# Performance work log

Measured on AMD Instinct MI355X. Metric: run time of the kernel, lower is better.

Reference implementation:

```python
import jax, jax.numpy as jnp
import numpy as np
import math

HIDDEN = 768
NUM_HEADS = 12
HEAD_DIM = HIDDEN // NUM_HEADS
EPS = 1e-05
MU_LEARNED = 0.0    # registered buffer init value (inference mode)
SIGMA_LEARNED = 1.0 # registered buffer init value (inference mode)
SCALES = (0.5, 1.0, 2.0)


def make_pe(n, d):
    # Sinusoidal positional encoding, identical to PositionalEncoding buffer.
    pos = np.arange(n, dtype=np.float32)[:, None]
    div = np.exp(np.arange(0, d, 2, dtype=np.float32) * (-math.log(10000.0) / d))
    pe = np.zeros((n, d), dtype=np.float32)
    pe[:, 0::2] = np.sin(pos * div)
    pe[:, 1::2] = np.cos(pos * div)
    return jnp.asarray(pe)


def setup_inputs() -> dict:
    key = jax.random.key(0)
    ks = jax.random.split(key, 12)
    B, C, Hh, Ww = 8, 256, 32, 32
    feat = jax.random.normal(ks[0], (B, C, Hh, Ww), jnp.float32)
    I = jax.random.uniform(ks[1], (B, 1, Hh, Ww), jnp.float32)
    sc_c = 1.0 / math.sqrt(C)
    sd = 1.0 / math.sqrt(HIDDEN)
    proj_w = jax.random.normal(ks[2], (C, HIDDEN), jnp.float32) * sc_c  # 1x1 conv as matmul
    proj_b = jnp.zeros((HIDDEN,), jnp.float32)
    wq = jax.random.normal(ks[3], (HIDDEN, HIDDEN), jnp.float32) * sd
    bq = jnp.zeros((HIDDEN,), jnp.float32)
    wk = jax.random.normal(ks[4], (HIDDEN, HIDDEN), jnp.float32) * sd
    bk = jnp.zeros((HIDDEN,), jnp.float32)
    wv = jax.random.normal(ks[5], (HIDDEN, HIDDEN), jnp.float32) * sd
    bv = jnp.zeros((HIDDEN,), jnp.float32)
    wo = jax.random.normal(ks[6], (HIDDEN, HIDDEN), jnp.float32) * sd
    bo = jnp.zeros((HIDDEN,), jnp.float32)
    lam = jnp.float32(0.5)
    return dict(feat=feat, I=I, proj_w=proj_w, proj_b=proj_b,
                wq=wq, bq=bq, wk=wk, bk=bk, wv=wv, bv=bv, wo=wo, bo=bo, lam=lam)


def reference(feat, I, proj_w, proj_b, wq, bq, wk, bk, wv, bv, wo, bo, lam):
    B, C, Hh, Ww = feat.shape
    N = Hh * Ww
    # HiddenFeatureProjection: 1x1 conv projection -> flatten -> tokens [B, N, D]
    tokens = jnp.einsum('bchw,cd->bhwd', feat, proj_w).reshape(B, N, HIDDEN) + proj_b
    tokens = tokens + make_pe(N, HIDDEN)[None]
    # GaussianWeightModule (inference path, learned buffers mu=0, sigma=1)
    G = sum(jnp.exp(-(I - MU_LEARNED) ** 2 / (2.0 * (k * SIGMA_LEARNED) ** 2 + EPS))
            for k in SCALES) / float(len(SCALES))  # [B,1,H,W]
    g = G.reshape(B, N)                              # H*W == N by construction
    bias = g[:, :, None] * g[:, None, :]             # [B, N, N] outer product
    # GaussianEnhancedAttention
    q = (tokens @ wq + bq).reshape(B, N, NUM_HEADS, HEAD_DIM).transpose(0, 2, 1, 3)
    k = (tokens @ wk + bk).reshape(B, N, NUM_HEADS, HEAD_DIM).transpose(0, 2, 1, 3)
    v = (tokens @ wv + bv).reshape(B, N, NUM_HEADS, HEAD_DIM).transpose(0, 2, 1, 3)
    scores = jnp.einsum('bhnd,bhmd->bhnm', q, k) / math.sqrt(HEAD_DIM)
    scores = scores + lam * bias[:, None, :, :]
    attn = jax.nn.softmax(scores, axis=-1)
    out = jnp.einsum('bhnm,bhmd->bhnd', attn, v).transpose(0, 2, 1, 3).reshape(B, N, HIDDEN)
    return out @ wo + bo
```

## Files before the change

kernel.cpp:

```cpp
#include <hip/hip_runtime.h>
#include <hip/hip_bf16.h>
#include <math.h>

#define HIDDEN 768
#define NHEADS 12
#define HDIM   64
#define NTOK   1024
#define BATCH  8
#define CIN    256
#define M_ALL  (BATCH * NTOK)
#define LSTR   72

typedef __hip_bfloat16 bf16;
typedef short frag8 __attribute__((ext_vector_type(8)));
typedef float f32x4 __attribute__((ext_vector_type(4)));

#define GL2LDS(gp, lp) \
    __builtin_amdgcn_global_load_lds((const __attribute__((address_space(1))) void*)(gp), \
                                     (__attribute__((address_space(3))) void*)(lp), 16, 0, 0)

__device__ __forceinline__ short f2bs(float x){
    union { bf16 h; short s; } u; u.h = __float2bfloat16(x); return u.s;
}

__device__ __forceinline__ float gaussw(float x){
    float x2 = x * x;
    return (__expf(-x2 / 0.50001f) + __expf(-x2 / 2.00001f) + __expf(-x2 / 8.00001f)) * (1.0f / 3.0f);
}

__global__ __launch_bounds__(256) void prep_all(
    const float* __restrict__ wq, const float* __restrict__ wk,
    const float* __restrict__ wv, const float* __restrict__ wo,
    const float* __restrict__ proj_w, const float* __restrict__ feat,
    short* __restrict__ wtqkv, short* __restrict__ wtp, short* __restrict__ featT)
{
    __shared__ short t[64][65];
    const int blk = blockIdx.x;
    const float* W; short* WT; int K, N, k0, n0;
    if (blk < 576) {
        int p = blk / 144, rem = blk % 144;
        const float* srcs[4] = {wq, wk, wv, wo};
        W = srcs[p]; WT = wtqkv + (size_t)p * HIDDEN * HIDDEN;
        K = HIDDEN; N = HIDDEN; k0 = (rem / 12) * 64; n0 = (rem % 12) * 64;
    } else if (blk < 624) {
        int rem = blk - 576;
        W = proj_w; WT = wtp;
        K = CIN; N = HIDDEN; k0 = (rem / 12) * 64; n0 = (rem % 12) * 64;
    } else {
        int rem = blk - 624;
        int b = rem / 64; rem %= 64;
        W = feat + (size_t)b * CIN * NTOK; WT = featT + (size_t)b * NTOK * CIN;
        K = CIN; N = NTOK; k0 = (rem / 16) * 64; n0 = (rem % 16) * 64;
    }
    const int tid = threadIdx.x;
    #pragma unroll
    for (int it = 0; it < 16; it++) {
        int e = tid + 256 * it;
        int kk = e / 64, nn = e % 64;
        t[kk][nn] = f2bs(W[(size_t)(k0 + kk) * N + n0 + nn]);
    }
    __syncthreads();
    #pragma unroll
    for (int it = 0; it < 16; it++) {
        int e = tid + 256 * it;
        int nn = e / 64, kk = e % 64;
        WT[(size_t)(n0 + nn) * K + k0 + kk] = t[kk][nn];
    }
}

__global__ __launch_bounds__(256) void transpose_v(
    const short* __restrict__ v, short* __restrict__ vT)
{
    __shared__ short t[64][65];
    const int nt = blockIdx.x;
    const int bh = blockIdx.y;
    const int b = bh / NHEADS, h = bh % NHEADS;
    const int tid = threadIdx.x;
    #pragma unroll
    for (int it = 0; it < 16; it++) {
        int e = tid + 256 * it;
        int rr = e / 64, cc = e % 64;
        t[rr][cc] = v[(size_t)(b * NTOK + nt * 64 + rr) * HIDDEN + h * HDIM + cc];
    }
    __syncthreads();
    #pragma unroll
    for (int it = 0; it < 16; it++) {
        int e = tid + 256 * it;
        int c2 = e / 64, r2 = e % 64;
        vT[((size_t)bh * HDIM + c2) * NTOK + nt * 64 + r2] = t[r2][c2];
    }
}

__global__ __launch_bounds__(256) void gemm_mfma128(
    const short* __restrict__ A, const short* __restrict__ WT0, long wt_z,
    const float* __restrict__ b0, const float* __restrict__ b1, const float* __restrict__ b2,
    short* o0, short* o1, short* o2, int K)
{
    __shared__ short Al[128 * 32];
    __shared__ short Bl[128 * 32];
    const int z = blockIdx.z;
    const short* WT  = WT0 + (size_t)z * wt_z;
    const float* bias = (z == 0) ? b0 : (z == 1) ? b1 : b2;
    short* outv       = (z == 0) ? o0 : (z == 1) ? o1 : o2;

    const int tid  = threadIdx.x;
    const int m0   = blockIdx.x * 128;
    const int n0   = blockIdx.y * 128;
    const int lane = tid & 63, wid = tid >> 6;
    const int wm   = (wid >> 1) * 64, wn = (wid & 1) * 64;
    const int l16  = lane & 15, quad = lane >> 4;

    const int sr  = lane >> 2;
    const int ssg = (lane & 3) ^ ((sr >> 1) & 3);
    const int fsw = (l16 >> 1) & 3;

    const f32x4 z4 = {0.f, 0.f, 0.f, 0.f};
    f32x4 acc[4][4];
    #pragma unroll
    for (int i = 0; i < 4; i++)
        #pragma unroll
        for (int j = 0; j < 4; j++) acc[i][j] = z4;

    for (int k0 = 0; k0 < K; k0 += 32) {
        #pragma unroll
        for (int t = 0; t < 2; t++) {
            int rbase = wid * 32 + t * 16;
            int r = rbase + sr;
            GL2LDS(A  + (size_t)(m0 + r) * K + k0 + ssg * 8, &Al[rbase * 32]);
            GL2LDS(WT + (size_t)(n0 + r) * K + k0 + ssg * 8, &Bl[rbase * 32]);
        }
        __syncthreads();
        frag8 af[4], bfr[4];
        #pragma unroll
        for (int i = 0; i < 4; i++)
            af[i]  = *(const frag8*)&Al[(wm + i * 16 + l16) * 32 + ((quad ^ fsw) * 8)];
        #pragma unroll
        for (int j = 0; j < 4; j++)
            bfr[j] = *(const frag8*)&Bl[(wn + j * 16 + l16) * 32 + ((quad ^ fsw) * 8)];
        #pragma unroll
        for (int i = 0; i < 4; i++)
            #pragma unroll
            for (int j = 0; j < 4; j++)
                acc[i][j] = __builtin_amdgcn_mfma_f32_16x16x32_bf16(af[i], bfr[j], acc[i][j], 0, 0, 0);
        __syncthreads();
    }

    #pragma unroll
    for (int i = 0; i < 4; i++) {
        #pragma unroll
        for (int r = 0; r < 4; r++) {
            int m = m0 + wm + i * 16 + quad * 4 + r;
            #pragma unroll
            for (int j = 0; j < 4; j++) {
                int col = n0 + wn + j * 16 + l16;
                outv[(size_t)m * HIDDEN + col] = f2bs(acc[i][j][r] + bias[col]);
            }
        }
    }
}

template<int MODE>
__global__ __launch_bounds__(256) void gemm_mfma64(
    const short* __restrict__ A, const short* __restrict__ WT,
    const float* __restrict__ bias, void* outv, int K)
{
    __shared__ short Al[64 * 32];
    __shared__ short Bl[128 * 32];
    const int tid  = threadIdx.x;
    const int m0   = blockIdx.x * 64;
    const int n0   = blockIdx.y * 128;
    const int lane = tid & 63, wid = tid >> 6;
    const int wn   = wid * 32;
    const int l16  = lane & 15, quad = lane >> 4;

    const int sr  = lane >> 2;
    const int ssg = (lane & 3) ^ ((sr >> 1) & 3);
    const int fsw = (l16 >> 1) & 3;

    const f32x4 z4 = {0.f, 0.f, 0.f, 0.f};
    f32x4 acc[4][2];
    #pragma unroll
    for (int i = 0; i < 4; i++)
        #pragma unroll
        for (int j = 0; j < 2; j++) acc[i][j] = z4;

    for (int k0 = 0; k0 < K; k0 += 32) {
        GL2LDS(A + (size_t)(m0 + wid * 16 + sr) * K + k0 + ssg * 8, &Al[(wid * 16) * 32]);
        #pragma unroll
        for (int t = 0; t < 2; t++) {
            int rbase = wid * 32 + t * 16;
            GL2LDS(WT + (size_t)(n0 + rbase + sr) * K + k0 + ssg * 8, &Bl[rbase * 32]);
        }
        __syncthreads();
        frag8 af[4], bfr[2];
        #pragma unroll
        for (int i = 0; i < 4; i++)
            af[i]  = *(const frag8*)&Al[(i * 16 + l16) * 32 + ((quad ^ fsw) * 8)];
        #pragma unroll
        for (int j = 0; j < 2; j++)
            bfr[j] = *(const frag8*)&Bl[(wn + j * 16 + l16) * 32 + ((quad ^ fsw) * 8)];
        #pragma unroll
        for (int i = 0; i < 4; i++)
            #pragma unroll
            for (int j = 0; j < 2; j++)
                acc[i][j] = __builtin_amdgcn_mfma_f32_16x16x32_bf16(af[i], bfr[j], acc[i][j], 0, 0, 0);
        __syncthreads();
    }

    const float kfac = -9.210340371976184f / 768.0f;
    #pragma unroll
    for (int i = 0; i < 4; i++) {
        #pragma unroll
        for (int r = 0; r < 4; r++) {
            int m = m0 + i * 16 + quad * 4 + r;
            #pragma unroll
            for (int j = 0; j < 2; j++) {
                int col = n0 + wn + j * 16 + l16;
                float val = acc[i][j][r] + bias[col];
                if (MODE == 1) {
                    int n_tok = m & (NTOK - 1);
                    float ang = (float)n_tok * expf((float)(2 * (col >> 1)) * kfac);
                    val += (col & 1) ? cosf(ang) : sinf(ang);
                }
                if (MODE == 2) ((float*)outv)[(size_t)m * HIDDEN + col] = val;
                else           ((short*)outv)[(size_t)m * HIDDEN + col] = f2bs(val);
            }
        }
    }
}

__global__ __launch_bounds__(256, 3) void attn_mfma(
    const short* __restrict__ q, const short* __restrict__ k, const short* __restrict__ vT,
    const float* __restrict__ I, const float* __restrict__ lam_p, short* __restrict__ out)
{
    __shared__ short QP[128 * LSTR];
    __shared__ short Ks[64 * 64];
    __shared__ short Vt[64 * 64];
    __shared__ float gL[NTOK];

    const int tid  = threadIdx.x;
    const int lin  = blockIdx.x;
    const int xcd  = lin & 7, slot = lin >> 3;
    const int b    = xcd;
    const int h    = slot >> 3;
    const int qt   = slot & 7;
    const float L2E  = 1.4426950408889634f;
    const float lam2 = lam_p[0] * L2E;
    const float scl  = 0.125f * L2E;
    const int lane = tid & 63, wave = tid >> 6;
    const int l16  = lane & 15, quad = lane >> 4;

    const int sr   = lane >> 3;
    const int slin = lane & 7;
    const int ssg  = slin ^ sr;
    const int fsw  = l16 & 7;

    for (int i = tid; i < NTOK; i += 256) gL[i] = gaussw(I[b * NTOK + i]);

    #pragma unroll
    for (int it = 0; it < 4; it++) {
        int e = tid + 256 * it;
        int r = e >> 3, seg = e & 7;
        *(frag8*)&QP[r * LSTR + seg * 8] =
            *(const frag8*)&q[(size_t)(b * NTOK + qt * 128 + r) * HIDDEN + h * HDIM + seg * 8];
    }
    __syncthreads();

    frag8 aq[2][2];
    #pragma unroll
    for (int half = 0; half < 2; half++) {
        aq[half][0] = *(const frag8*)&QP[(wave * 32 + half * 16 + l16) * LSTR + quad * 8];
        aq[half][1] = *(const frag8*)&QP[(wave * 32 + half * 16 + l16) * LSTR + 32 + quad * 8];
    }
    float gi[2][4];
    #pragma unroll
    for (int half = 0; half < 2; half++)
        #pragma unroll
        for (int r = 0; r < 4; r++)
            gi[half][r] = gL[qt * 128 + wave * 32 + half * 16 + quad * 4 + r];

    const f32x4 z4 = {0.f, 0.f, 0.f, 0.f};
    f32x4 o_acc[2][4];
    #pragma unroll
    for (int half = 0; half < 2; half++)
        #pragma unroll
        for (int d = 0; d < 4; d++) o_acc[half][d] = z4;
    float l_run[2][4] = {};

    const size_t kb  = (size_t)b * NTOK * HIDDEN + h * HDIM;
    const size_t vtb = (size_t)(b * NHEADS + h) * HDIM * NTOK;

    for (int jt = 0; jt < 16; jt++) {
        __syncthreads();
        #pragma unroll
        for (int t = 0; t < 2; t++) {
            int rbase = wave * 16 + t * 8;
            int r = rbase + sr;
            GL2LDS(k  + kb  + (size_t)(jt * 64 + r) * HIDDEN + ssg * 8, &Ks[rbase * 64]);
            GL2LDS(vT + vtb + (size_t)r * NTOK + jt * 64 + ssg * 8,     &Vt[rbase * 64]);
        }
        __syncthreads();

        float p[2][4][4];
        #pragma unroll
        for (int t4 = 0; t4 < 4; t4++) {
            frag8 bk0 = *(const frag8*)&Ks[(t4 * 16 + l16) * 64 + ((quad ^ fsw) * 8)];
            frag8 bk1 = *(const frag8*)&Ks[(t4 * 16 + l16) * 64 + (((quad + 4) ^ fsw) * 8)];
            #pragma unroll
            for (int half = 0; half < 2; half++) {
                f32x4 a = z4;
                a = __builtin_amdgcn_mfma_f32_16x16x32_bf16(aq[half][0], bk0, a, 0, 0, 0);
                a = __builtin_amdgcn_mfma_f32_16x16x32_bf16(aq[half][1], bk1, a, 0, 0, 0);
                #pragma unroll
                for (int r = 0; r < 4; r++) p[half][t4][r] = a[r];
            }
        }

        float gjs[4];
        #pragma unroll
        for (int t4 = 0; t4 < 4; t4++) gjs[t4] = lam2 * gL[jt * 64 + t4 * 16 + l16];

        #pragma unroll
        for (int half = 0; half < 2; half++)
            #pragma unroll
            for (int t4 = 0; t4 < 4; t4++)
                #pragma unroll
                for (int r = 0; r < 4; r++) {
                    float e = exp2f(p[half][t4][r] * scl + gi[half][r] * gjs[t4]);
                    l_run[half][r] += e;
                    QP[(wave * 32 + half * 16 + quad * 4 + r) * LSTR + t4 * 16 + l16] = f2bs(e);
                }

        frag8 ap[2][2];
        #pragma unroll
        for (int half = 0; half < 2; half++) {
            ap[half][0] = *(const frag8*)&QP[(wave * 32 + half * 16 + l16) * LSTR + quad * 8];
            ap[half][1] = *(const frag8*)&QP[(wave * 32 + half * 16 + l16) * LSTR + 32 + quad * 8];
        }
        #pragma unroll
        for (int d = 0; d < 4; d++) {
            frag8 bv0 = *(const frag8*)&Vt[(d * 16 + l16) * 64 + ((quad ^ fsw) * 8)];
            frag8 bv1 = *(const frag8*)&Vt[(d * 16 + l16) * 64 + (((quad + 4) ^ fsw) * 8)];
            #pragma unroll
            for (int half = 0; half < 2; half++) {
                o_acc[half][d] = __builtin_amdgcn_mfma_f32_16x16x32_bf16(ap[half][0], bv0, o_acc[half][d], 0, 0, 0);
                o_acc[half][d] = __builtin_amdgcn_mfma_f32_16x16x32_bf16(ap[half][1], bv1, o_acc[half][d], 0, 0, 0);
            }
        }
    }

    #pragma unroll
    for (int half = 0; half < 2; half++)
        #pragma unroll
        for (int r = 0; r < 4; r++) {
            float l = l_run[half][r];
            #pragma unroll
            for (int off = 1; off < 16; off <<= 1) l += __shfl_xor(l, off);
            float inv_l = 1.0f / l;
            int row = qt * 128 + wave * 32 + half * 16 + quad * 4 + r;
            #pragma unroll
            for (int d = 0; d < 4; d++)
                out[(size_t)(b * NTOK + row) * HIDDEN + h * HDIM + d * 16 + l16]
                    = f2bs(o_acc[half][d][r] * inv_l);
        }
}

extern "C" void kernel_launch(void* const* d_in, const int* in_sizes, int n_in,
                              void* d_out, int out_size, void* d_ws, size_t ws_size,
                              hipStream_t stream)
{
    const float* feat   = (const float*)d_in[0];
    const float* I      = (const float*)d_in[1];
    const float* proj_w = (const float*)d_in[2];
    const float* proj_b = (const float*)d_in[3];
    const float* wq     = (const float*)d_in[4];
    const float* bq     = (const float*)d_in[5];
    const float* wk     = (const float*)d_in[6];
    const float* bk     = (const float*)d_in[7];
    const float* wv     = (const float*)d_in[8];
    const float* bv     = (const float*)d_in[9];
    const float* wo     = (const float*)d_in[10];
    const float* bo     = (const float*)d_in[11];
    const float* lam    = (const float*)d_in[12];
    float* out = (float*)d_out;

    short* wtqkv = (short*)d_ws;
    short* wto   = wtqkv + (size_t)3 * HIDDEN * HIDDEN;
    short* wtp   = wto   + (size_t)HIDDEN * HIDDEN;
    short* tokens= wtp   + (size_t)HIDDEN * CIN;
    short* qbuf  = tokens+ (size_t)M_ALL * HIDDEN;
    short* featT = qbuf;
    short* vTb   = tokens;
    short* kbuf  = (short*)d_out;
    short* vbuf  = kbuf + (size_t)M_ALL * HIDDEN;

    prep_all<<<1136, 256, 0, stream>>>(wq, wk, wv, wo, proj_w, feat, wtqkv, wtp, featT);
    gemm_mfma64<1><<<dim3(128, 6), 256, 0, stream>>>(featT, wtp, proj_b, tokens, CIN);
    gemm_mfma128<<<dim3(64, 6, 3), 256, 0, stream>>>(tokens, wtqkv, (long)HIDDEN * HIDDEN,
                                                     bq, bk, bv,
                                                     qbuf, kbuf, vbuf, HIDDEN);
    transpose_v<<<dim3(16, 96), 256, 0, stream>>>(vbuf, vTb);
    attn_mfma<<<768, 256, 0, stream>>>(qbuf, kbuf, vTb, I, lam, qbuf);
    gemm_mfma64<2><<<dim3(128, 6), 256, 0, stream>>>(qbuf, wto, bo, out, HIDDEN);
}
```

Measured before the change: 239.8 us.

## Double-buffer K/V tiles in attention and precompute Gaussian weights

```diff
diff --git a/kernel.cpp b/kernel.cpp
--- a/kernel.cpp
+++ b/kernel.cpp
@@ -13,6 +13,7 @@
 
 typedef __hip_bfloat16 bf16;
 typedef short frag8 __attribute__((ext_vector_type(8)));
+typedef short s16x4 __attribute__((ext_vector_type(4)));
 typedef float f32x4 __attribute__((ext_vector_type(4)));
 
 #define GL2LDS(gp, lp) \
@@ -69,8 +70,15 @@
 }
 
 __global__ __launch_bounds__(256) void transpose_v(
-    const short* __restrict__ v, short* __restrict__ vT)
-{
+    const short* __restrict__ v, short* __restrict__ vT,
+    const float* __restrict__ I, float* __restrict__ g)
+{
+    if (blockIdx.y == BATCH * NHEADS) {
+        int idx = blockIdx.x * 512 + threadIdx.x * 2;
+        g[idx]     = gaussw(I[idx]);
+        g[idx + 1] = gaussw(I[idx + 1]);
+        return;
+    }
     __shared__ short t[64][65];
     const int nt = blockIdx.x;
     const int bh = blockIdx.y;
@@ -231,12 +239,11 @@
 
 __global__ __launch_bounds__(256, 3) void attn_mfma(
     const short* __restrict__ q, const short* __restrict__ k, const short* __restrict__ vT,
-    const float* __restrict__ I, const float* __restrict__ lam_p, short* __restrict__ out)
-{
-    __shared__ short QP[128 * LSTR];
-    __shared__ short Ks[64 * 64];
-    __shared__ short Vt[64 * 64];
-    __shared__ float gL[NTOK];
+    const float* __restrict__ g, const float* __restrict__ lam_p, short* __restrict__ out)
+{
+    __shared__ short Pl[128 * LSTR];
+    __shared__ short Ks[2][64 * 64];
+    __shared__ short Vt[2][64 * 64];
 
     const int tid  = threadIdx.x;
     const int lin  = blockIdx.x;
@@ -255,29 +262,30 @@
     const int ssg  = slin ^ sr;
     const int fsw  = l16 & 7;
 
-    for (int i = tid; i < NTOK; i += 256) gL[i] = gaussw(I[b * NTOK + i]);
-
-    #pragma unroll
-    for (int it = 0; it < 4; it++) {
-        int e = tid + 256 * it;
-        int r = e >> 3, seg = e & 7;
-        *(frag8*)&QP[r * LSTR + seg * 8] =
-            *(const frag8*)&q[(size_t)(b * NTOK + qt * 128 + r) * HIDDEN + h * HDIM + seg * 8];
+    const size_t kb  = (size_t)b * NTOK * HIDDEN + h * HDIM;
+    const size_t vtb = (size_t)(b * NHEADS + h) * HDIM * NTOK;
+    const float* gk  = g + b * NTOK;
+
+    frag8 aq[2][2];
+    #pragma unroll
+    for (int half = 0; half < 2; half++)
+        #pragma unroll
+        for (int kc = 0; kc < 2; kc++)
+            aq[half][kc] = *(const frag8*)&q[(size_t)(b * NTOK + qt * 128 + wave * 32 + half * 16 + l16) * HIDDEN
+                                             + h * HDIM + kc * 32 + quad * 8];
+    float gq[2];
+    #pragma unroll
+    for (int half = 0; half < 2; half++)
+        gq[half] = lam2 * gk[qt * 128 + wave * 32 + half * 16 + l16];
+
+    #pragma unroll
+    for (int t = 0; t < 2; t++) {
+        int rbase = wave * 16 + t * 8;
+        int r = rbase + sr;
+        GL2LDS(k  + kb  + (size_t)r * HIDDEN + ssg * 8,  &Ks[0][rbase * 64]);
+        GL2LDS(vT + vtb + (size_t)r * NTOK + ssg * 8,    &Vt[0][rbase * 64]);
     }
     __syncthreads();
-
-    frag8 aq[2][2];
-    #pragma unroll
-    for (int half = 0; half < 2; half++) {
-        aq[half][0] = *(const frag8*)&QP[(wave * 32 + half * 16 + l16) * LSTR + quad * 8];
-        aq[half][1] = *(const frag8*)&QP[(wave * 32 + half * 16 + l16) * LSTR + 32 + quad * 8];
-    }
-    float gi[2][4];
-    #pragma unroll
-    for (int half = 0; half < 2; half++)
-        #pragma unroll
-        for (int r = 0; r < 4; r++)
-            gi[half][r] = gL[qt * 128 + wave * 32 + half * 16 + quad * 4 + r];
 
     const f32x4 z4 = {0.f, 0.f, 0.f, 0.f};
     f32x4 o_acc[2][4];
@@ -285,84 +293,88 @@
     for (int half = 0; half < 2; half++)
         #pragma unroll
         for (int d = 0; d < 4; d++) o_acc[half][d] = z4;
-    float l_run[2][4] = {};
-
-    const size_t kb  = (size_t)b * NTOK * HIDDEN + h * HDIM;
-    const size_t vtb = (size_t)(b * NHEADS + h) * HDIM * NTOK;
+    float l_run[2] = {0.f, 0.f};
 
     for (int jt = 0; jt < 16; jt++) {
-        __syncthreads();
-        #pragma unroll
-        for (int t = 0; t < 2; t++) {
-            int rbase = wave * 16 + t * 8;
-            int r = rbase + sr;
-            GL2LDS(k  + kb  + (size_t)(jt * 64 + r) * HIDDEN + ssg * 8, &Ks[rbase * 64]);
-            GL2LDS(vT + vtb + (size_t)r * NTOK + jt * 64 + ssg * 8,     &Vt[rbase * 64]);
-        }
-        __syncthreads();
+        const int cur = jt & 1;
+        if (jt < 15) {
+            #pragma unroll
+            for (int t = 0; t < 2; t++) {
+                int rbase = wave * 16 + t * 8;
+                int r = rbase + sr;
+                GL2LDS(k  + kb  + (size_t)((jt + 1) * 64 + r) * HIDDEN + ssg * 8, &Ks[cur ^ 1][rbase * 64]);
+                GL2LDS(vT + vtb + (size_t)r * NTOK + (jt + 1) * 64 + ssg * 8,     &Vt[cur ^ 1][rbase * 64]);
+            }
+        }
+        f32x4 gk4[4];
+        #pragma unroll
+        for (int t4 = 0; t4 < 4; t4++)
+            gk4[t4] = *(const f32x4*)&gk[jt * 64 + t4 * 16 + quad * 4];
 
         float p[2][4][4];
         #pragma unroll
         for (int t4 = 0; t4 < 4; t4++) {
-            frag8 bk0 = *(const frag8*)&Ks[(t4 * 16 + l16) * 64 + ((quad ^ fsw) * 8)];
-            frag8 bk1 = *(const frag8*)&Ks[(t4 * 16 + l16) * 64 + (((quad + 4) ^ fsw) * 8)];
+            frag8 ak0 = *(const frag8*)&Ks[cur][(t4 * 16 + l16) * 64 + ((quad ^ fsw) * 8)];
+            frag8 ak1 = *(const frag8*)&Ks[cur][(t4 * 16 + l16) * 64 + (((quad + 4) ^ fsw) * 8)];
             #pragma unroll
             for (int half = 0; half < 2; half++) {
                 f32x4 a = z4;
-                a = __builtin_amdgcn_mfma_f32_16x16x32_bf16(aq[half][0], bk0, a, 0, 0, 0);
-                a = __builtin_amdgcn_mfma_f32_16x16x32_bf16(aq[half][1], bk1, a, 0, 0, 0);
+                a = __builtin_amdgcn_mfma_f32_16x16x32_bf16(ak0, aq[half][0], a, 0, 0, 0);
+                a = __builtin_amdgcn_mfma_f32_16x16x32_bf16(ak1, aq[half][1], a, 0, 0, 0);
                 #pragma unroll
                 for (int r = 0; r < 4; r++) p[half][t4][r] = a[r];
             }
         }
 
-        float gjs[4];
-        #pragma unroll
-        for (int t4 = 0; t4 < 4; t4++) gjs[t4] = lam2 * gL[jt * 64 + t4 * 16 + l16];
-
         #pragma unroll
         for (int half = 0; half < 2; half++)
             #pragma unroll
-            for (int t4 = 0; t4 < 4; t4++)
+            for (int t4 = 0; t4 < 4; t4++) {
+                s16x4 w;
                 #pragma unroll
                 for (int r = 0; r < 4; r++) {
-                    float e = exp2f(p[half][t4][r] * scl + gi[half][r] * gjs[t4]);
-                    l_run[half][r] += e;
-                    QP[(wave * 32 + half * 16 + quad * 4 + r) * LSTR + t4 * 16 + l16] = f2bs(e);
+                    float e = exp2f(p[half][t4][r] * scl + gq[half] * gk4[t4][r]);
+                    l_run[half] += e;
+                    w[r] = f2bs(e);
                 }
+                *(s16x4*)&Pl[(wave * 32 + half * 16 + l16) * LSTR + t4 * 16 + quad * 4] = w;
+            }
 
         frag8 ap[2][2];
         #pragma unroll
-        for (int half = 0; half < 2; half++) {
-            ap[half][0] = *(const frag8*)&QP[(wave * 32 + half * 16 + l16) * LSTR + quad * 8];
-            ap[half][1] = *(const frag8*)&QP[(wave * 32 + half * 16 + l16) * LSTR + 32 + quad * 8];
-        }
+        for (int half = 0; half < 2; half++)
+            #pragma unroll
+            for (int kc = 0; kc < 2; kc++)
+                ap[half][kc] = *(const frag8*)&Pl[(wave * 32 + half * 16 + l16) * LSTR + kc * 32 + quad * 8];
         #pragma unroll
         for (int d = 0; d < 4; d++) {
-            frag8 bv0 = *(const frag8*)&Vt[(d * 16 + l16) * 64 + ((quad ^ fsw) * 8)];
-            frag8 bv1 = *(const frag8*)&Vt[(d * 16 + l16) * 64 + (((quad + 4) ^ fsw) * 8)];
+            frag8 av0 = *(const frag8*)&Vt[cur][(d * 16 + l16) * 64 + ((quad ^ fsw) * 8)];
+            frag8 av1 = *(const frag8*)&Vt[cur][(d * 16 + l16) * 64 + (((quad + 4) ^ fsw) * 8)];
             #pragma unroll
             for (int half = 0; half < 2; half++) {
-                o_acc[half][d] = __builtin_amdgcn_mfma_f32_16x16x32_bf16(ap[half][0], bv0, o_acc[half][d], 0, 0, 0);
-                o_acc[half][d] = __builtin_amdgcn_mfma_f32_16x16x32_bf16(ap[half][1], bv1, o_acc[half][d], 0, 0, 0);
-            }
-        }
-    }
-
-    #pragma unroll
-    for (int half = 0; half < 2; half++)
+                o_acc[half][d] = __builtin_amdgcn_mfma_f32_16x16x32_bf16(ap[half][0], av0, o_acc[half][d], 0, 0, 0);
+                o_acc[half][d] = __builtin_amdgcn_mfma_f32_16x16x32_bf16(ap[half][1], av1, o_acc[half][d], 0, 0, 0);
+            }
+        }
+        __syncthreads();
+    }
+
+    #pragma unroll
+    for (int half = 0; half < 2; half++) {
+        float l = l_run[half];
+        l += __shfl_xor(l, 16);
+        l += __shfl_xor(l, 32);
         #pragma unroll
         for (int r = 0; r < 4; r++) {
-            float l = l_run[half][r];
-            #pragma unroll
-            for (int off = 1; off < 16; off <<= 1) l += __shfl_xor(l, off);
-            float inv_l = 1.0f / l;
+            float lq = __shfl(l, (lane & 48) | (quad * 4 + r));
+            float inv_l = 1.0f / lq;
             int row = qt * 128 + wave * 32 + half * 16 + quad * 4 + r;
             #pragma unroll
             for (int d = 0; d < 4; d++)
                 out[(size_t)(b * NTOK + row) * HIDDEN + h * HDIM + d * 16 + l16]
                     = f2bs(o_acc[half][d][r] * inv_l);
         }
+    }
 }
 
 extern "C" void kernel_launch(void* const* d_in, const int* in_sizes, int n_in,
@@ -393,13 +405,14 @@
     short* vTb   = tokens;
     short* kbuf  = (short*)d_out;
     short* vbuf  = kbuf + (size_t)M_ALL * HIDDEN;
+    float* gbuf  = (float*)wtp;
 
     prep_all<<<1136, 256, 0, stream>>>(wq, wk, wv, wo, proj_w, feat, wtqkv, wtp, featT);
     gemm_mfma64<1><<<dim3(128, 6), 256, 0, stream>>>(featT, wtp, proj_b, tokens, CIN);
     gemm_mfma128<<<dim3(64, 6, 3), 256, 0, stream>>>(tokens, wtqkv, (long)HIDDEN * HIDDEN,
                                                      bq, bk, bv,
                                                      qbuf, kbuf, vbuf, HIDDEN);
-    transpose_v<<<dim3(16, 96), 256, 0, stream>>>(vbuf, vTb);
-    attn_mfma<<<768, 256, 0, stream>>>(qbuf, kbuf, vTb, I, lam, qbuf);
+    transpose_v<<<dim3(16, 97), 256, 0, stream>>>(vbuf, vTb, I, gbuf);
+    attn_mfma<<<768, 256, 0, stream>>>(qbuf, kbuf, vTb, gbuf, lam, qbuf);
     gemm_mfma64<2><<<dim3(128, 6), 256, 0, stream>>>(qbuf, wto, bo, out, HIDDEN);
 }
```

Result: no change. 237.7 us (-0.9%).
